# Optimization experiments

Hardware: AMD Instinct MI355X
Metric: run time of the kernel (lower is better)

Reference implementation:

```python
import jax, jax.numpy as jnp
import numpy as np

D_MODEL = 1024
B, T = 4, 2048
LN_EPS = 1e-5


def setup_inputs() -> dict:
    key = jax.random.key(0)
    ks = jax.random.split(key, 8)
    d = D_MODEL
    x = jax.random.normal(ks[0], (B, T, d), dtype=jnp.float32)
    # linear params (fan-in scaled)
    W_in = jax.random.normal(ks[1], (d, 4 * d), dtype=jnp.float32) / np.sqrt(d)
    b_in = jnp.zeros((4 * d,), dtype=jnp.float32)
    W_out = jax.random.normal(ks[2], (2 * d, d), dtype=jnp.float32) / np.sqrt(2 * d)
    b_out = jnp.zeros((d,), dtype=jnp.float32)
    # LRU initializer (matches the torch module's initializer())
    rng = np.random.default_rng(0)
    r_min, r_max = 0.9, 0.999
    u1 = rng.random(d)
    u2 = rng.random(d)
    nu_log = np.log(-0.5 * np.log(u1 * (r_max ** 2 - r_min ** 2) + r_min ** 2))
    theta_log = np.log(u2 * np.pi * 2)
    gamma_log = np.log(np.sqrt(1 - np.exp(-np.exp(nu_log)) ** 2))
    # LayerNorm affine params
    ln_w = jnp.ones((2 * d,), dtype=jnp.float32)
    ln_b = jnp.zeros((2 * d,), dtype=jnp.float32)
    return {
        "x": x,
        "W_in": W_in, "b_in": b_in,
        "nu_log": jnp.asarray(nu_log, dtype=jnp.float32),
        "theta_log": jnp.asarray(theta_log, dtype=jnp.float32),
        "gamma_log": jnp.asarray(gamma_log, dtype=jnp.float32),
        "ln_w": ln_w, "ln_b": ln_b,
        "W_out": W_out, "b_out": b_out,
    }


def _complex_scan(in_r, in_i, f_r, f_i):
    """h_t = f * h_{t-1} + in_t over axis=1, complex math in real/imag pairs."""
    def combine(l, r):
        a1r, a1i, b1r, b1i = l
        a2r, a2i, b2r, b2i = r
        ar = a2r * a1r - a2i * a1i
        ai = a2r * a1i + a2i * a1r
        br = a2r * b1r - a2i * b1i + b2r
        bi = a2r * b1i + a2i * b1r + b2i
        return (ar, ai, br, bi)
    fr = jnp.broadcast_to(f_r, in_r.shape)
    fi = jnp.broadcast_to(f_i, in_i.shape)
    _, _, hr, hi = jax.lax.associative_scan(combine, (fr, fi, in_r, in_i), axis=1)
    return hr, hi


def reference(x, W_in, b_in, nu_log, theta_log, gamma_log, ln_w, ln_b, W_out, b_out):
    d = x.shape[-1]
    u = x @ W_in + b_in                       # [B, T, 4d]
    v, o = u[..., :2 * d], u[..., 2 * d:]     # each [B, T, 2d]
    nu = jnp.exp(-jnp.exp(nu_log))            # [d]
    theta = jnp.exp(theta_log)
    gamma = jnpp_exp = jnp.exp(gamma_log)
    f_r = nu * jnp.cos(theta)
    f_i = nu * jnp.sin(theta)
    in_r = gamma * v[..., :d]                 # [B, T, d]
    in_i = gamma * v[..., d:]
    h_r, h_i = _complex_scan(in_r, in_i, f_r, f_i)
    y = jnp.concatenate([h_r, h_i], axis=-1) * jax.nn.silu(o)  # [B, T, 2d]
    mu = jnp.mean(y, axis=-1, keepdims=True)
    var = jnp.mean(jnp.square(y - mu), axis=-1, keepdims=True)
    y = (y - mu) * jax.lax.rsqrt(var + LN_EPS) * ln_w + ln_b
    return y @ W_out + b_out                  # [B, T, d]
```

## Files before the change

### kernel.cpp

```cpp
#include <hip/hip_runtime.h>
#include <hip/hip_bf16.h>

#define D_MODEL 1024
#define BB 4
#define TT 2048
#define ROWS (BB*TT)
#define NCHUNK 32
#define CHLEN 64

typedef __attribute__((ext_vector_type(8))) short short8;
typedef __attribute__((ext_vector_type(4))) float floatx4;

static __device__ __forceinline__ ushort f2bf(float f) {
    union { float f; unsigned u; } v; v.f = f;
    unsigned r = v.u + 0x7FFF + ((v.u >> 16) & 1);
    return (ushort)(r >> 16);
}
static __device__ __forceinline__ float bf2f(ushort b) {
    union { unsigned u; float f; } v; v.u = ((unsigned)b) << 16;
    return v.f;
}

#define GLOAD_LDS16(gp, lp)                                                 \
    __builtin_amdgcn_global_load_lds(                                       \
        (const __attribute__((address_space(1))) void*)(gp),                \
        (__attribute__((address_space(3))) void*)(lp), 16, 0, 0)

#define PREP_A 8192
#define PREP_B 4096
#define PREP_C 2048
__global__ __launch_bounds__(256) void prep_all(
    const float* __restrict__ x, ushort* __restrict__ xb,
    const float* __restrict__ W_in, ushort* __restrict__ WinT,
    const float* __restrict__ W_out, ushort* __restrict__ W1T,
    const float* __restrict__ lnw, const float* __restrict__ lnb,
    float* __restrict__ s1, float* __restrict__ c2,
    const float* __restrict__ nu_log, const float* __restrict__ theta_log,
    const float* __restrict__ gamma_log,
    float* __restrict__ fr, float* __restrict__ fi, float* __restrict__ gm) {
    __shared__ float smem[32 * 33 + 8 * 32 * 2];
    int bid = blockIdx.x, tid = threadIdx.x;
    if (bid < PREP_A) {
        int i = bid * 256 + tid;
        float4 v = ((const float4*)x)[i];
        ushort4 o;
        o.x = f2bf(v.x); o.y = f2bf(v.y); o.z = f2bf(v.z); o.w = f2bf(v.w);
        ((ushort4*)xb)[i] = o;
    } else if (bid < PREP_A + PREP_B) {
        int b2 = bid - PREP_A;
        int n0 = (b2 & 127) * 32, k0 = (b2 >> 7) * 32;
        int tx = tid & 31, ty = tid >> 5;
        float (*tile)[33] = (float (*)[33])smem;
#pragma unroll
        for (int j = 0; j < 4; ++j)
            tile[ty + j*8][tx] = W_in[(size_t)(k0 + ty + j*8) * 4096 + n0 + tx];
        __syncthreads();
#pragma unroll
        for (int j = 0; j < 4; ++j)
            WinT[(size_t)(n0 + ty + j*8) * 1024 + k0 + tx] = f2bf(tile[tx][ty + j*8]);
    } else if (bid < PREP_A + PREP_B + PREP_C) {
        int b2 = bid - PREP_A - PREP_B;
        int n0 = (b2 & 31) * 32, k0 = (b2 >> 5) * 32;
        int tx = tid & 31, ty = tid >> 5;
        float (*tile)[33] = (float (*)[33])smem;
        float* red1 = smem + 32 * 33;
        float* red2 = red1 + 8 * 32;
        float p1 = 0.f, p2 = 0.f;
#pragma unroll
        for (int j = 0; j < 4; ++j) {
            int k = k0 + ty + j * 8;
            float w = W_out[(size_t)k * 1024 + n0 + tx];
            float lw = lnw[k], lb = lnb[k];
            tile[ty + j*8][tx] = lw * w;
            p1 += lw * w; p2 += lb * w;
        }
        __syncthreads();
#pragma unroll
        for (int j = 0; j < 4; ++j)
            W1T[(size_t)(n0 + ty + j*8) * 2048 + k0 + tx] = f2bf(tile[tx][ty + j*8]);
        red1[ty * 32 + tx] = p1; red2[ty * 32 + tx] = p2;
        __syncthreads();
        if (ty == 0) {
            float a = 0.f, b = 0.f;
#pragma unroll
            for (int t = 0; t < 8; ++t) { a += red1[t * 32 + tx]; b += red2[t * 32 + tx]; }
            atomicAdd(&s1[n0 + tx], a);
            atomicAdd(&c2[n0 + tx], b);
        }
    } else {
        int c = (bid - PREP_A - PREP_B - PREP_C) * 256 + tid;
        if (c < D_MODEL) {
            float nu = expf(-expf(nu_log[c]));
            float th = expf(theta_log[c]);
            fr[c] = nu * cosf(th);
            fi[c] = nu * sinf(th);
            gm[c] = expf(gamma_log[c]);
        }
    }
}

__global__ __launch_bounds__(256) void gemm_bf16(
    const ushort* __restrict__ A, const ushort* __restrict__ B,
    int K, int N, const float* __restrict__ bias, int mode,
    const float* __restrict__ gamma,
    ushort* __restrict__ out_r, ushort* __restrict__ out_i,
    ushort* __restrict__ out_o, float* __restrict__ outC,
    const float* __restrict__ mu, const float* __restrict__ rs,
    const float* __restrict__ s1, const float* __restrict__ c2) {
    __shared__ ushort As[128 * 64];
    __shared__ ushort Bs[128 * 64];
    int tid = threadIdx.x;
    int lane = tid & 63, wave = tid >> 6;
    int wm = (wave & 1) * 64, wn = (wave >> 1) * 64;
    int lr = lane & 15, q = lane >> 4;
    long m0 = (long)blockIdx.y * 128;
    long n0 = (long)blockIdx.x * 128;
    floatx4 acc[4][4] = {};

    int rs_ = tid >> 3;
    int pg = ((tid & 7) ^ (rs_ & 7)) * 8;
    const ushort* Ap = A + (m0 + rs_) * (long)K + pg;
    const ushort* Bp = B + (n0 + rs_) * (long)K + pg;
    int swl = lr & 7;

    for (int kt = 0; kt < K; kt += 64) {
        __syncthreads();
#pragma unroll
        for (int j = 0; j < 4; ++j) {
            GLOAD_LDS16(Ap + kt + (long)(j * 32) * K, &As[(j * 256 + tid) * 8]);
            GLOAD_LDS16(Bp + kt + (long)(j * 32) * K, &Bs[(j * 256 + tid) * 8]);
        }
        __syncthreads();
#pragma unroll
        for (int s = 0; s < 2; ++s) {
            short8 af[4], bfv[4];
            int pq = ((s * 4 + q) ^ swl) * 8;
#pragma unroll
            for (int r = 0; r < 4; ++r)
                af[r] = *(const short8*)&As[(wm + r * 16 + lr) * 64 + pq];
#pragma unroll
            for (int c = 0; c < 4; ++c)
                bfv[c] = *(const short8*)&Bs[(wn + c * 16 + lr) * 64 + pq];
#pragma unroll
            for (int r = 0; r < 4; ++r)
#pragma unroll
                for (int c = 0; c < 4; ++c)
                    acc[r][c] = __builtin_amdgcn_mfma_f32_16x16x32_bf16(
                        af[r], bfv[c], acc[r][c], 0, 0, 0);
        }
    }

    if (mode == 2) {
#pragma unroll
        for (int r = 0; r < 4; ++r) {
#pragma unroll
            for (int c = 0; c < 4; ++c) {
                long col = n0 + wn + c * 16 + lr;
                float bc = c2[col] + bias[col];
                float s1c = s1[col];
#pragma unroll
                for (int g = 0; g < 4; ++g) {
                    long row = m0 + wm + r * 16 + q * 4 + g;
                    outC[row * (long)N + col] =
                        rs[row] * (acc[r][c][g] - mu[row] * s1c) + bc;
                }
            }
        }
    } else {
        int sector = (int)((n0 + wn) >> 10);
        int lc0 = (int)((n0 + wn) & 1023);
        if (sector < 2) {
            ushort* dst = sector ? out_i : out_r;
#pragma unroll
            for (int r = 0; r < 4; ++r) {
#pragma unroll
                for (int c = 0; c < 4; ++c) {
                    int lc = lc0 + c * 16 + lr;
                    float bv = bias[(sector << 10) + lc];
                    float gv = gamma[lc];
#pragma unroll
                    for (int g = 0; g < 4; ++g) {
                        long row = m0 + wm + r * 16 + q * 4 + g;
                        dst[row * 1024 + lc] = f2bf(gv * (acc[r][c][g] + bv));
                    }
                }
            }
        } else {
            int oc0 = (int)(n0 + wn - 2048);
#pragma unroll
            for (int r = 0; r < 4; ++r) {
#pragma unroll
                for (int c = 0; c < 4; ++c) {
                    int oc = oc0 + c * 16 + lr;
                    float bv = bias[2048 + oc];
#pragma unroll
                    for (int g = 0; g < 4; ++g) {
                        long row = m0 + wm + r * 16 + q * 4 + g;
                        out_o[row * 2048 + oc] = f2bf(acc[r][c][g] + bv);
                    }
                }
            }
        }
    }
}

__global__ __launch_bounds__(256) void scan_carries(
    const ushort* __restrict__ in_r, const ushort* __restrict__ in_i,
    float* __restrict__ carry,
    const float* __restrict__ fr_, const float* __restrict__ fi_) {
    int t = blockIdx.x * 256 + threadIdx.x;
    int c = t & 1023;
    int ck = (t >> 10) & (NCHUNK - 1);
    int b = t >> 15;
    float fr = fr_[c], fi = fi_[c];
    size_t base = ((size_t)(b * TT + ck * CHLEN)) * 1024 + c;
    float hr = 0.f, hi = 0.f;
#pragma unroll 4
    for (int j = 0; j < CHLEN; ++j) {
        size_t idx = base + (size_t)j * 1024;
        float r = bf2f(in_r[idx]), im = bf2f(in_i[idx]);
        float nhr = fr * hr - fi * hi + r;
        float nhi = fr * hi + fi * hr + im;
        hr = nhr; hi = nhi;
    }
    size_t ci = (((size_t)b * 1024 + c) * NCHUNK + ck) * 2;
    carry[ci] = hr; carry[ci + 1] = hi;
}

__global__ __launch_bounds__(256) void scan_apply(
    const ushort* __restrict__ in_r, const ushort* __restrict__ in_i,
    const float* __restrict__ carry,
    const float* __restrict__ fr_, const float* __restrict__ fi_,
    const ushort* __restrict__ o, ushort* __restrict__ yb) {
    int t = blockIdx.x * 256 + threadIdx.x;
    int c = t & 1023;
    int ck = (t >> 10) & (NCHUNK - 1);
    int b = t >> 15;
    float fr = fr_[c], fi = fi_[c];
    float ar = fr, ai = fi;
#pragma unroll
    for (int s = 0; s < 6; ++s) {
        float nr = ar * ar - ai * ai, ni = 2.f * ar * ai;
        ar = nr; ai = ni;
    }
    float Hr = 0.f, Hi = 0.f;
    size_t cb = ((size_t)b * 1024 + c) * NCHUNK * 2;
    for (int k = 0; k < ck; ++k) {
        float cr = carry[cb + k * 2], cim = carry[cb + k * 2 + 1];
        float nHr = ar * Hr - ai * Hi + cr;
        float nHi = ar * Hi + ai * Hr + cim;
        Hr = nHr; Hi = nHi;
    }
    size_t base = ((size_t)(b * TT + ck * CHLEN)) * 1024 + c;
    size_t rowbase = (size_t)(b * TT + ck * CHLEN);
    float hr = Hr, hi = Hi;
#pragma unroll 2
    for (int j = 0; j < CHLEN; ++j) {
        size_t idx = base + (size_t)j * 1024;
        float r = bf2f(in_r[idx]), im = bf2f(in_i[idx]);
        float nhr = fr * hr - fi * hi + r;
        float nhi = fr * hi + fi * hr + im;
        hr = nhr; hi = nhi;
        size_t ob = (rowbase + j) * 2048 + c;
        float ov1 = bf2f(o[ob]);
        float ov2 = bf2f(o[ob + 1024]);
        float y1 = hr * ov1 / (1.f + __expf(-ov1));
        float y2 = hi * ov2 / (1.f + __expf(-ov2));
        yb[ob] = f2bf(y1);
        yb[ob + 1024] = f2bf(y2);
    }
}

__global__ __launch_bounds__(256) void row_stats(
    const ushort* __restrict__ yb, float* __restrict__ mu_o,
    float* __restrict__ rs_o) {
    long row = blockIdx.x;
    int tid = threadIdx.x;
    const ushort* p = yb + row * 2048 + tid * 8;
    uint4 raw = *(const uint4*)p;
    float s = 0.f, s2 = 0.f;
    unsigned w[4] = {raw.x, raw.y, raw.z, raw.w};
#pragma unroll
    for (int j = 0; j < 4; ++j) {
        float a = bf2f((ushort)(w[j] & 0xffff));
        float b = bf2f((ushort)(w[j] >> 16));
        s += a + b; s2 += a * a + b * b;
    }
#pragma unroll
    for (int off = 32; off > 0; off >>= 1) {
        s += __shfl_down(s, off, 64);
        s2 += __shfl_down(s2, off, 64);
    }
    __shared__ float red[8];
    int wv = tid >> 6;
    if ((tid & 63) == 0) { red[wv] = s; red[4 + wv] = s2; }
    __syncthreads();
    if (tid == 0) {
        s = red[0] + red[1] + red[2] + red[3];
        s2 = red[4] + red[5] + red[6] + red[7];
        float mu = s * (1.f / 2048.f);
        float var = s2 * (1.f / 2048.f) - mu * mu;
        mu_o[row] = mu;
        rs_o[row] = rsqrtf(var + 1e-5f);
    }
}


extern "C" void kernel_launch(void* const* d_in, const int* in_sizes, int n_in,
                              void* d_out, int out_size, void* d_ws, size_t ws_size,
                              hipStream_t stream) {
    const float* x         = (const float*)d_in[0];
    const float* W_in      = (const float*)d_in[1];
    const float* b_in      = (const float*)d_in[2];
    const float* nu_log    = (const float*)d_in[3];
    const float* theta_log = (const float*)d_in[4];
    const float* gamma_log = (const float*)d_in[5];
    const float* ln_w      = (const float*)d_in[6];
    const float* ln_b      = (const float*)d_in[7];
    const float* W_out     = (const float*)d_in[8];
    const float* b_out     = (const float*)d_in[9];
    float* out = (float*)d_out;

    char* ws = (char*)d_ws;
    size_t off = 0;
    auto alloc = [&](size_t bytes) {
        char* p = ws + off;
        off += (bytes + 255) & ~(size_t)255;
        return p;
    };
    ushort* xb    = (ushort*)alloc((size_t)ROWS * 1024 * 2);
    ushort* WinT  = (ushort*)alloc((size_t)4096 * 1024 * 2);
    ushort* W1T   = (ushort*)alloc((size_t)1024 * 2048 * 2);
    float*  fr    = (float*)alloc(1024 * 4);
    float*  fi    = (float*)alloc(1024 * 4);
    float*  gm    = (float*)alloc(1024 * 4);
    float*  s1c2  = (float*)alloc(2048 * 4);
    float*  s1    = s1c2;
    float*  c2    = s1c2 + 1024;
    ushort* in_r  = (ushort*)alloc((size_t)ROWS * 1024 * 2);
    ushort* in_i  = (ushort*)alloc((size_t)ROWS * 1024 * 2);
    ushort* obuf  = (ushort*)alloc((size_t)ROWS * 2048 * 2);
    float*  carry = (float*)alloc((size_t)BB * 1024 * NCHUNK * 2 * 4);
    ushort* yb    = (ushort*)alloc((size_t)ROWS * 2048 * 2);
    float*  muv   = (float*)alloc(ROWS * 4);
    float*  rsv   = (float*)alloc(ROWS * 4);

    hipMemsetAsync(s1c2, 0, 2048 * 4, stream);

    prep_all<<<PREP_A + PREP_B + PREP_C + 4, 256, 0, stream>>>(
        x, xb, W_in, WinT, W_out, W1T, ln_w, ln_b, s1, c2,
        nu_log, theta_log, gamma_log, fr, fi, gm);

    gemm_bf16<<<dim3(4096 / 128, ROWS / 128), 256, 0, stream>>>(
        xb, WinT, 1024, 4096, b_in, 1, gm, in_r, in_i, obuf, nullptr,
        nullptr, nullptr, nullptr, nullptr);

    scan_carries<<<BB * 1024 * NCHUNK / 256, 256, 0, stream>>>(in_r, in_i, carry, fr, fi);
    scan_apply<<<BB * 1024 * NCHUNK / 256, 256, 0, stream>>>(
        in_r, in_i, carry, fr, fi, obuf, yb);

    row_stats<<<ROWS, 256, 0, stream>>>(yb, muv, rsv);

    gemm_bf16<<<dim3(1024 / 128, ROWS / 128), 256, 0, stream>>>(
        yb, W1T, 2048, 1024, b_out, 2, nullptr, nullptr, nullptr, nullptr, out,
        muv, rsv, s1, c2);
}
```

Baseline: 296.8 us.

## Fuse row statistics into scan apply via atomics and vectorize scan over channel pairs

Removes the separate row_stats kernel: scan_apply now accumulates per-row sum and sum of squares with wave reductions and atomicAdd, and the output GEMM epilogue derives mean and rstd from those sums. The scan kernels process two channels per thread with 32-bit loads, use a channel-contiguous carry layout in separate real and imaginary arrays, and switch to 64 chunks of 32 steps. This cuts one full read of the y buffer and increases scan parallelism. In exchange it adds many atomics (eight per row per chunk block) and an extra memset of the sum buffers, and the float atomics make the accumulation order nondeterministic.

After: 306.4 us. +3.2%, slower.

```diff
diff --git a/kernel.cpp b/kernel.cpp
--- a/kernel.cpp
+++ b/kernel.cpp
@@ -5,8 +5,8 @@
 #define BB 4
 #define TT 2048
 #define ROWS (BB*TT)
-#define NCHUNK 32
-#define CHLEN 64
+#define NCHUNK 64
+#define CHLEN 32
 
 typedef __attribute__((ext_vector_type(8))) short short8;
 typedef __attribute__((ext_vector_type(4))) float floatx4;
@@ -19,6 +19,9 @@
 static __device__ __forceinline__ float bf2f(ushort b) {
     union { unsigned u; float f; } v; v.u = ((unsigned)b) << 16;
     return v.f;
+}
+static __device__ __forceinline__ float silu(float x) {
+    return x / (1.f + __expf(-x));
 }
 
 #define GLOAD_LDS16(gp, lp)                                                 \
@@ -105,7 +108,7 @@
     const float* __restrict__ gamma,
     ushort* __restrict__ out_r, ushort* __restrict__ out_i,
     ushort* __restrict__ out_o, float* __restrict__ outC,
-    const float* __restrict__ mu, const float* __restrict__ rs,
+    const float* __restrict__ ssum, const float* __restrict__ s2sum,
     const float* __restrict__ s1, const float* __restrict__ c2) {
     __shared__ ushort As[128 * 64];
     __shared__ ushort Bs[128 * 64];
@@ -151,6 +154,18 @@
     }
 
     if (mode == 2) {
+        float muv[4][4], rsvv[4][4];
+#pragma unroll
+        for (int r = 0; r < 4; ++r)
+#pragma unroll
+            for (int g = 0; g < 4; ++g) {
+                long row = m0 + wm + r * 16 + q * 4 + g;
+                float sv = ssum[row], s2v = s2sum[row];
+                float m = sv * (1.f / 2048.f);
+                float var = s2v * (1.f / 2048.f) - m * m;
+                muv[r][g] = m;
+                rsvv[r][g] = rsqrtf(var + 1e-5f);
+            }
 #pragma unroll
         for (int r = 0; r < 4; ++r) {
 #pragma unroll
@@ -162,7 +177,7 @@
                 for (int g = 0; g < 4; ++g) {
                     long row = m0 + wm + r * 16 + q * 4 + g;
                     outC[row * (long)N + col] =
-                        rs[row] * (acc[r][c][g] - mu[row] * s1c) + bc;
+                        rsvv[r][g] * (acc[r][c][g] - muv[r][g] * s1c) + bc;
                 }
             }
         }
@@ -206,102 +221,103 @@
 
 __global__ __launch_bounds__(256) void scan_carries(
     const ushort* __restrict__ in_r, const ushort* __restrict__ in_i,
-    float* __restrict__ carry,
+    float* __restrict__ carry_r, float* __restrict__ carry_i,
     const float* __restrict__ fr_, const float* __restrict__ fi_) {
     int t = blockIdx.x * 256 + threadIdx.x;
-    int c = t & 1023;
-    int ck = (t >> 10) & (NCHUNK - 1);
+    int ch2 = t & 511;
+    int ck = (t >> 9) & (NCHUNK - 1);
     int b = t >> 15;
-    float fr = fr_[c], fi = fi_[c];
+    int c = ch2 * 2;
+    float fr0 = fr_[c], fi0 = fi_[c];
+    float fr1 = fr_[c + 1], fi1 = fi_[c + 1];
     size_t base = ((size_t)(b * TT + ck * CHLEN)) * 1024 + c;
-    float hr = 0.f, hi = 0.f;
+    float h0r = 0.f, h0i = 0.f, h1r = 0.f, h1i = 0.f;
 #pragma unroll 4
     for (int j = 0; j < CHLEN; ++j) {
         size_t idx = base + (size_t)j * 1024;
-        float r = bf2f(in_r[idx]), im = bf2f(in_i[idx]);
-        float nhr = fr * hr - fi * hi + r;
-        float nhi = fr * hi + fi * hr + im;
-        hr = nhr; hi = nhi;
-    }
-    size_t ci = (((size_t)b * 1024 + c) * NCHUNK + ck) * 2;
-    carry[ci] = hr; carry[ci + 1] = hi;
+        unsigned rr = *(const unsigned*)(in_r + idx);
+        unsigned ii = *(const unsigned*)(in_i + idx);
+        float r0 = bf2f((ushort)(rr & 0xffff)), r1 = bf2f((ushort)(rr >> 16));
+        float i0 = bf2f((ushort)(ii & 0xffff)), i1 = bf2f((ushort)(ii >> 16));
+        float n0r = fr0 * h0r - fi0 * h0i + r0;
+        float n0i = fr0 * h0i + fi0 * h0r + i0;
+        float n1r = fr1 * h1r - fi1 * h1i + r1;
+        float n1i = fr1 * h1i + fi1 * h1r + i1;
+        h0r = n0r; h0i = n0i; h1r = n1r; h1i = n1i;
+    }
+    size_t ci = ((size_t)(b * NCHUNK + ck)) * 1024 + c;
+    *(float2*)&carry_r[ci] = make_float2(h0r, h1r);
+    *(float2*)&carry_i[ci] = make_float2(h0i, h1i);
 }
 
 __global__ __launch_bounds__(256) void scan_apply(
     const ushort* __restrict__ in_r, const ushort* __restrict__ in_i,
-    const float* __restrict__ carry,
+    const float* __restrict__ carry_r, const float* __restrict__ carry_i,
     const float* __restrict__ fr_, const float* __restrict__ fi_,
-    const ushort* __restrict__ o, ushort* __restrict__ yb) {
-    int t = blockIdx.x * 256 + threadIdx.x;
-    int c = t & 1023;
-    int ck = (t >> 10) & (NCHUNK - 1);
-    int b = t >> 15;
-    float fr = fr_[c], fi = fi_[c];
-    float ar = fr, ai = fi;
-#pragma unroll
-    for (int s = 0; s < 6; ++s) {
-        float nr = ar * ar - ai * ai, ni = 2.f * ar * ai;
-        ar = nr; ai = ni;
-    }
-    float Hr = 0.f, Hi = 0.f;
-    size_t cb = ((size_t)b * 1024 + c) * NCHUNK * 2;
+    const ushort* __restrict__ o, ushort* __restrict__ yb,
+    float* __restrict__ ssum, float* __restrict__ s2sum) {
+    int ck = blockIdx.x;
+    int by = blockIdx.y;
+    int b = by >> 1, half = by & 1;
+    int tid = threadIdx.x;
+    int ch2 = half * 256 + tid;
+    int c = ch2 * 2;
+    float fr0 = fr_[c], fi0 = fi_[c];
+    float fr1 = fr_[c + 1], fi1 = fi_[c + 1];
+    float a0r = fr0, a0i = fi0, a1r = fr1, a1i = fi1;
+#pragma unroll
+    for (int s = 0; s < 5; ++s) {
+        float t0r = a0r * a0r - a0i * a0i, t0i = 2.f * a0r * a0i;
+        float t1r = a1r * a1r - a1i * a1i, t1i = 2.f * a1r * a1i;
+        a0r = t0r; a0i = t0i; a1r = t1r; a1i = t1i;
+    }
+    float H0r = 0.f, H0i = 0.f, H1r = 0.f, H1i = 0.f;
+    size_t cb = ((size_t)(b * NCHUNK)) * 1024 + c;
     for (int k = 0; k < ck; ++k) {
-        float cr = carry[cb + k * 2], cim = carry[cb + k * 2 + 1];
-        float nHr = ar * Hr - ai * Hi + cr;
-        float nHi = ar * Hi + ai * Hr + cim;
-        Hr = nHr; Hi = nHi;
-    }
-    size_t base = ((size_t)(b * TT + ck * CHLEN)) * 1024 + c;
+        float2 crv = *(const float2*)&carry_r[cb + (size_t)k * 1024];
+        float2 civ = *(const float2*)&carry_i[cb + (size_t)k * 1024];
+        float n0r = a0r * H0r - a0i * H0i + crv.x;
+        float n0i = a0r * H0i + a0i * H0r + civ.x;
+        float n1r = a1r * H1r - a1i * H1i + crv.y;
+        float n1i = a1r * H1i + a1i * H1r + civ.y;
+        H0r = n0r; H0i = n0i; H1r = n1r; H1i = n1i;
+    }
     size_t rowbase = (size_t)(b * TT + ck * CHLEN);
-    float hr = Hr, hi = Hi;
+    float h0r = H0r, h0i = H0i, h1r = H1r, h1i = H1i;
 #pragma unroll 2
     for (int j = 0; j < CHLEN; ++j) {
-        size_t idx = base + (size_t)j * 1024;
-        float r = bf2f(in_r[idx]), im = bf2f(in_i[idx]);
-        float nhr = fr * hr - fi * hi + r;
-        float nhi = fr * hi + fi * hr + im;
-        hr = nhr; hi = nhi;
-        size_t ob = (rowbase + j) * 2048 + c;
-        float ov1 = bf2f(o[ob]);
-        float ov2 = bf2f(o[ob + 1024]);
-        float y1 = hr * ov1 / (1.f + __expf(-ov1));
-        float y2 = hi * ov2 / (1.f + __expf(-ov2));
-        yb[ob] = f2bf(y1);
-        yb[ob + 1024] = f2bf(y2);
-    }
-}
-
-__global__ __launch_bounds__(256) void row_stats(
-    const ushort* __restrict__ yb, float* __restrict__ mu_o,
-    float* __restrict__ rs_o) {
-    long row = blockIdx.x;
-    int tid = threadIdx.x;
-    const ushort* p = yb + row * 2048 + tid * 8;
-    uint4 raw = *(const uint4*)p;
-    float s = 0.f, s2 = 0.f;
-    unsigned w[4] = {raw.x, raw.y, raw.z, raw.w};
-#pragma unroll
-    for (int j = 0; j < 4; ++j) {
-        float a = bf2f((ushort)(w[j] & 0xffff));
-        float b = bf2f((ushort)(w[j] >> 16));
-        s += a + b; s2 += a * a + b * b;
-    }
-#pragma unroll
-    for (int off = 32; off > 0; off >>= 1) {
-        s += __shfl_down(s, off, 64);
-        s2 += __shfl_down(s2, off, 64);
-    }
-    __shared__ float red[8];
-    int wv = tid >> 6;
-    if ((tid & 63) == 0) { red[wv] = s; red[4 + wv] = s2; }
-    __syncthreads();
-    if (tid == 0) {
-        s = red[0] + red[1] + red[2] + red[3];
-        s2 = red[4] + red[5] + red[6] + red[7];
-        float mu = s * (1.f / 2048.f);
-        float var = s2 * (1.f / 2048.f) - mu * mu;
-        mu_o[row] = mu;
-        rs_o[row] = rsqrtf(var + 1e-5f);
+        size_t row = rowbase + j;
+        size_t idx = row * 1024 + c;
+        unsigned rr = *(const unsigned*)(in_r + idx);
+        unsigned ii = *(const unsigned*)(in_i + idx);
+        unsigned oo1 = *(const unsigned*)(o + row * 2048 + c);
+        unsigned oo2 = *(const unsigned*)(o + row * 2048 + c + 1024);
+        float r0 = bf2f((ushort)(rr & 0xffff)), r1 = bf2f((ushort)(rr >> 16));
+        float i0 = bf2f((ushort)(ii & 0xffff)), i1 = bf2f((ushort)(ii >> 16));
+        float n0r = fr0 * h0r - fi0 * h0i + r0;
+        float n0i = fr0 * h0i + fi0 * h0r + i0;
+        float n1r = fr1 * h1r - fi1 * h1i + r1;
+        float n1i = fr1 * h1i + fi1 * h1r + i1;
+        h0r = n0r; h0i = n0i; h1r = n1r; h1i = n1i;
+        float o0 = bf2f((ushort)(oo1 & 0xffff)), o1 = bf2f((ushort)(oo1 >> 16));
+        float o2 = bf2f((ushort)(oo2 & 0xffff)), o3 = bf2f((ushort)(oo2 >> 16));
+        float y0 = h0r * silu(o0), y1 = h1r * silu(o1);
+        float y2 = h0i * silu(o2), y3 = h1i * silu(o3);
+        *(unsigned*)(yb + row * 2048 + c) =
+            (unsigned)f2bf(y0) | ((unsigned)f2bf(y1) << 16);
+        *(unsigned*)(yb + row * 2048 + c + 1024) =
+            (unsigned)f2bf(y2) | ((unsigned)f2bf(y3) << 16);
+        float s = y0 + y1 + y2 + y3;
+        float s2 = y0 * y0 + y1 * y1 + y2 * y2 + y3 * y3;
+#pragma unroll
+        for (int off = 32; off > 0; off >>= 1) {
+            s += __shfl_down(s, off, 64);
+            s2 += __shfl_down(s2, off, 64);
+        }
+        if ((tid & 63) == 0) {
+            atomicAdd(&ssum[row], s);
+            atomicAdd(&s2sum[row], s2);
+        }
     }
 }
 
@@ -334,18 +350,19 @@
     float*  fr    = (float*)alloc(1024 * 4);
     float*  fi    = (float*)alloc(1024 * 4);
     float*  gm    = (float*)alloc(1024 * 4);
-    float*  s1c2  = (float*)alloc(2048 * 4);
-    float*  s1    = s1c2;
-    float*  c2    = s1c2 + 1024;
+    float*  zbuf  = (float*)alloc((size_t)(2048 + 2 * ROWS) * 4);
+    float*  s1    = zbuf;
+    float*  c2    = zbuf + 1024;
+    float*  ssum  = zbuf + 2048;
+    float*  s2sum = zbuf + 2048 + ROWS;
     ushort* in_r  = (ushort*)alloc((size_t)ROWS * 1024 * 2);
     ushort* in_i  = (ushort*)alloc((size_t)ROWS * 1024 * 2);
     ushort* obuf  = (ushort*)alloc((size_t)ROWS * 2048 * 2);
-    float*  carry = (float*)alloc((size_t)BB * 1024 * NCHUNK * 2 * 4);
+    float*  car_r = (float*)alloc((size_t)BB * NCHUNK * 1024 * 4);
+    float*  car_i = (float*)alloc((size_t)BB * NCHUNK * 1024 * 4);
     ushort* yb    = (ushort*)alloc((size_t)ROWS * 2048 * 2);
-    float*  muv   = (float*)alloc(ROWS * 4);
-    float*  rsv   = (float*)alloc(ROWS * 4);
-
-    hipMemsetAsync(s1c2, 0, 2048 * 4, stream);
+
+    hipMemsetAsync(zbuf, 0, (size_t)(2048 + 2 * ROWS) * 4, stream);
 
     prep_all<<<PREP_A + PREP_B + PREP_C + 4, 256, 0, stream>>>(
         x, xb, W_in, WinT, W_out, W1T, ln_w, ln_b, s1, c2,
@@ -355,13 +372,12 @@
         xb, WinT, 1024, 4096, b_in, 1, gm, in_r, in_i, obuf, nullptr,
         nullptr, nullptr, nullptr, nullptr);
 
-    scan_carries<<<BB * 1024 * NCHUNK / 256, 256, 0, stream>>>(in_r, in_i, carry, fr, fi);
-    scan_apply<<<BB * 1024 * NCHUNK / 256, 256, 0, stream>>>(
-        in_r, in_i, carry, fr, fi, obuf, yb);
-
-    row_stats<<<ROWS, 256, 0, stream>>>(yb, muv, rsv);
+    scan_carries<<<BB * 512 * NCHUNK / 256, 256, 0, stream>>>(
+        in_r, in_i, car_r, car_i, fr, fi);
+    scan_apply<<<dim3(NCHUNK, BB * 2), 256, 0, stream>>>(
+        in_r, in_i, car_r, car_i, fr, fi, obuf, yb, ssum, s2sum);
 
     gemm_bf16<<<dim3(1024 / 128, ROWS / 128), 256, 0, stream>>>(
         yb, W1T, 2048, 1024, b_out, 2, nullptr, nullptr, nullptr, nullptr, out,
-        muv, rsv, s1, c2);
-}
+        ssum, s2sum, s1, c2);
+}
```
